# Kernel tuning notes

Hardware: AMD Instinct MI355X
Metric: run time of the kernel (lower is better)

Reference implementation:

```python
import jax, jax.numpy as jnp
import numpy as np

KSZ = 7
PAD = 3


def setup_inputs() -> dict:
    key = jax.random.key(0)
    ks = jax.random.split(key, 5)
    b, t, c, h, w = 8, 16, 256, 28, 28
    x = jax.random.normal(ks[0], (b, t, c, h, w), dtype=jnp.float32)
    W1 = jax.random.normal(ks[1], (2 * t, t), dtype=jnp.float32) * 0.1
    W2 = jax.random.normal(ks[2], (KSZ, 2 * t), dtype=jnp.float32) * 0.1
    Wl1 = jax.random.normal(ks[3], (c // 4, c, KSZ), dtype=jnp.float32) * 0.05
    Wl2 = jax.random.normal(ks[4], (c, c // 4, 1), dtype=jnp.float32) * 0.1
    return {"x": x, "W1": W1, "W2": W2, "Wl1": Wl1, "Wl2": Wl2}


def _tam_forward(x, W1, W2, Wl1, Wl2):
    b, t, c, h, w = x.shape
    xp = jnp.transpose(x, (0, 2, 1, 3, 4))  # [b,c,t,h,w]
    pooled = jnp.mean(xp, axis=(3, 4))       # [b,c,t] (adaptive_avg_pool2d to 1x1)

    # G branch: per-(b,c) dynamic 7-tap softmax kernel
    g = jnp.tanh(jnp.einsum('bct,ut->bcu', pooled, W1))
    kernel = jax.nn.softmax(jnp.einsum('bcu,ku->bck', g, W2), axis=-1)  # [b,c,7]

    # L branch: conv1d(c -> c/4, k=7, pad=3) -> tanh -> conv1d(c/4 -> c, k=1) -> sigmoid
    y = jax.lax.conv_general_dilated(
        pooled, Wl1, window_strides=(1,), padding=[(PAD, PAD)],
        dimension_numbers=('NCH', 'OIH', 'NCH'))
    y = jnp.tanh(y)  # [b, c/4, t]
    local = jax.nn.sigmoid(jnp.einsum('oi,bit->bot', Wl2[:, :, 0], y))  # [b,c,t]

    gated = xp * local[:, :, :, None, None]  # [b,c,t,h,w]

    # Depthwise temporal conv (groups = b*c), stride 1, pad 3 on t
    padded = jnp.pad(gated, ((0, 0), (0, 0), (PAD, PAD), (0, 0), (0, 0)))
    out = jnp.zeros_like(gated)
    for k in range(KSZ):
        out = out + kernel[:, :, k, None, None, None] * padded[:, :, k:k + t]
    out = jnp.transpose(out, (0, 2, 1, 3, 4))  # [b,t,c,h,w]
    return out.reshape(b * t, c, h, w)


def reference(x, W1, W2, Wl1, Wl2):
    return _tam_forward(x, W1, W2, Wl1, Wl2)
```

## Files before the change

### kernel.cpp

```cpp
#include <hip/hip_runtime.h>

constexpr int B_  = 8;
constexpr int T_  = 16;
constexpr int C_  = 256;
constexpr int HW_ = 784;
constexpr int CO_ = 64;
constexpr int K_  = 7;
constexpr int U2_ = 32;

typedef float floatx4 __attribute__((ext_vector_type(4)));

__global__ __launch_bounds__(256) void pool_kernel(const float* __restrict__ x,
                                                   float* __restrict__ pooled) {
    int bid  = blockIdx.x;
    int cg   = bid & 63;
    int bt   = bid >> 6;
    int t    = bt & 15;
    int b    = bt >> 4;
    int wave = threadIdx.x >> 6;
    int lane = threadIdx.x & 63;
    int c    = cg * 4 + wave;

    const float4* p4 = (const float4*)(x + ((size_t)bt * C_ + c) * HW_);
    float s = 0.f;
    for (int j = lane; j < 196; j += 64) {
        float4 v = p4[j];
        s += (v.x + v.y) + (v.z + v.w);
    }
#pragma unroll
    for (int m = 32; m >= 1; m >>= 1) s += __shfl_xor(s, m, 64);
    if (lane == 0) pooled[((size_t)b * C_ + c) * T_ + t] = s * (1.0f / 784.0f);
}

__global__ __launch_bounds__(256) void ty_kernel(const float* __restrict__ pooled,
                                                 const float* __restrict__ Wl1,
                                                 float* __restrict__ ty) {
    int b = blockIdx.x / CO_;
    int o = blockIdx.x % CO_;
    __shared__ float pld[T_ * 257];

    int tid = threadIdx.x;
    for (int idx = tid; idx < C_ * T_; idx += 256) {
        int i  = idx >> 4;
        int tt = idx & 15;
        pld[tt * 257 + i] = pooled[((size_t)b * C_ + i) * T_ + tt];
    }
    __syncthreads();

    int t = tid >> 4;
    int q = tid & 15;
    const float* wrow = Wl1 + (size_t)o * (C_ * K_);
    float acc = 0.f;
    for (int j = 0; j < 16; ++j) {
        int i = j * 16 + q;
        const float* wp = wrow + i * K_;
#pragma unroll
        for (int k = 0; k < K_; ++k) {
            int tt = t + k - 3;
            if (tt >= 0 && tt < T_) acc += wp[k] * pld[tt * 257 + i];
        }
    }
    acc += __shfl_xor(acc, 1, 64);
    acc += __shfl_xor(acc, 2, 64);
    acc += __shfl_xor(acc, 4, 64);
    acc += __shfl_xor(acc, 8, 64);
    if (q == 0) ty[((size_t)b * CO_ + o) * T_ + t] = tanhf(acc);
}

__global__ __launch_bounds__(64) void abuild_kernel(const float* __restrict__ pooled,
                                                    const float* __restrict__ ty,
                                                    const float* __restrict__ W1,
                                                    const float* __restrict__ W2,
                                                    const float* __restrict__ Wl2,
                                                    float* __restrict__ P) {
    int bc = blockIdx.x;
    int b  = bc >> 8;
    int c  = bc & 255;
    int lane = threadIdx.x;

    __shared__ float g_s[U2_];
    __shared__ float s_s[K_];
    __shared__ float loc_s[T_];
    __shared__ float kw_s[8];

    {
        int t = lane >> 2, q = lane & 3;
        float acc = 0.f;
#pragma unroll
        for (int jj = 0; jj < 16; ++jj) {
            int i = q * 16 + jj;
            acc += Wl2[(size_t)c * CO_ + i] * ty[((size_t)b * CO_ + i) * T_ + t];
        }
        acc += __shfl_xor(acc, 1, 64);
        acc += __shfl_xor(acc, 2, 64);
        if (q == 0) loc_s[t] = 1.0f / (1.0f + __expf(-acc));
    }
    if (lane < U2_) {
        float acc = 0.f;
#pragma unroll
        for (int t2 = 0; t2 < T_; ++t2)
            acc += pooled[((size_t)b * C_ + c) * T_ + t2] * W1[lane * T_ + t2];
        g_s[lane] = tanhf(acc);
    }
    __syncthreads();
    if (lane < K_) {
        float acc = 0.f;
#pragma unroll
        for (int u = 0; u < U2_; ++u) acc += g_s[u] * W2[lane * U2_ + u];
        s_s[lane] = acc;
    }
    __syncthreads();
    if (lane == 0) {
        float m = s_s[0];
#pragma unroll
        for (int k = 1; k < K_; ++k) m = fmaxf(m, s_s[k]);
        float e[K_], sum = 0.f;
#pragma unroll
        for (int k = 0; k < K_; ++k) { e[k] = __expf(s_s[k] - m); sum += e[k]; }
        float inv = 1.0f / sum;
#pragma unroll
        for (int k = 0; k < K_; ++k) kw_s[k] = e[k] * inv;
        kw_s[7] = 0.f;
    }
    __syncthreads();
    float* row = P + (size_t)bc * 32;
    if (lane < 8)                 row[lane] = kw_s[lane];
    if (lane >= 8 && lane < 24)   row[lane] = loc_s[lane - 8];
}

__global__ __launch_bounds__(256) void stream_kernel(const float* __restrict__ x,
                                                     const float* __restrict__ P,
                                                     float* __restrict__ out) {
    int gid = blockIdx.x * 256 + threadIdx.x;
    int bc  = gid / 196;
    int col = gid - bc * 196;
    int b   = bc >> 8;
    int c   = bc & 255;

    const float* row = P + (size_t)bc * 32;
    float4 kwa = *(const float4*)(row);
    float4 kwb = *(const float4*)(row + 4);
    float kw[K_] = {kwa.x, kwa.y, kwa.z, kwa.w, kwb.x, kwb.y, kwb.z};
    float loc[T_];
#pragma unroll
    for (int j = 0; j < 4; ++j) {
        float4 l = *(const float4*)(row + 8 + 4 * j);
        loc[4 * j + 0] = l.x; loc[4 * j + 1] = l.y;
        loc[4 * j + 2] = l.z; loc[4 * j + 3] = l.w;
    }

    size_t base = ((size_t)(b * T_) * C_ + c) * HW_ + (size_t)col * 4;
    const size_t ts = (size_t)C_ * HW_;

    float4 yv[T_];
#pragma unroll
    for (int tp = 0; tp < T_; ++tp) {
        float4 v = *(const float4*)(x + base + tp * ts);
        float l = loc[tp];
        v.x *= l; v.y *= l; v.z *= l; v.w *= l;
        yv[tp] = v;
    }
#pragma unroll
    for (int t = 0; t < T_; ++t) {
        floatx4 acc = {0.f, 0.f, 0.f, 0.f};
#pragma unroll
        for (int d = -3; d <= 3; ++d) {
            int tp = t + d;
            if (tp >= 0 && tp < T_) {
                float a = kw[d + 3];
                acc.x += a * yv[tp].x;
                acc.y += a * yv[tp].y;
                acc.z += a * yv[tp].z;
                acc.w += a * yv[tp].w;
            }
        }
        __builtin_nontemporal_store(acc, (floatx4*)(out + base + (size_t)t * ts));
    }
}

extern "C" void kernel_launch(void* const* d_in, const int* in_sizes, int n_in,
                              void* d_out, int out_size, void* d_ws, size_t ws_size,
                              hipStream_t stream) {
    const float* x   = (const float*)d_in[0];
    const float* W1  = (const float*)d_in[1];
    const float* W2  = (const float*)d_in[2];
    const float* Wl1 = (const float*)d_in[3];
    const float* Wl2 = (const float*)d_in[4];
    float* out = (float*)d_out;

    float* pooled = (float*)d_ws;
    float* ty     = pooled + B_ * C_ * T_;
    float* P      = ty + B_ * CO_ * T_;

    pool_kernel<<<B_ * T_ * (C_ / 4), 256, 0, stream>>>(x, pooled);
    ty_kernel<<<B_ * CO_, 256, 0, stream>>>(pooled, Wl1, ty);
    abuild_kernel<<<B_ * C_, 64, 0, stream>>>(pooled, ty, W1, W2, Wl2, P);
    stream_kernel<<<(B_ * C_ * 196) / 256, 256, 0, stream>>>(x, P, out);
}
```

Measured before the change: 72.72 us.

## Map one block per channel in stream kernel and split time loop into halves

The streaming kernel now launches one block per (b,c) channel, with 196 active threads out of 256. The per-channel kernel weights and gates are made wave-uniform via readfirstlane so they can sit in scalar registers. The 16-step register window is replaced by two overlapping 11-frame windows, which lowers vector register pressure, and launch bounds request higher occupancy. The cost is 60 idle lanes per block and some loads issued later, after the first half of the stores.

```diff
diff --git a/kernel.cpp b/kernel.cpp
--- a/kernel.cpp
+++ b/kernel.cpp
@@ -9,6 +9,10 @@
 constexpr int U2_ = 32;
 
 typedef float floatx4 __attribute__((ext_vector_type(4)));
+
+__device__ __forceinline__ float rfl(float v) {
+    return __int_as_float(__builtin_amdgcn_readfirstlane(__float_as_int(v)));
+}
 
 __global__ __launch_bounds__(256) void pool_kernel(const float* __restrict__ x,
                                                    float* __restrict__ pooled) {
@@ -128,53 +132,61 @@
     if (lane >= 8 && lane < 24)   row[lane] = loc_s[lane - 8];
 }
 
-__global__ __launch_bounds__(256) void stream_kernel(const float* __restrict__ x,
-                                                     const float* __restrict__ P,
-                                                     float* __restrict__ out) {
-    int gid = blockIdx.x * 256 + threadIdx.x;
-    int bc  = gid / 196;
-    int col = gid - bc * 196;
-    int b   = bc >> 8;
-    int c   = bc & 255;
+__global__ __launch_bounds__(256, 8) void stream_kernel(const float* __restrict__ x,
+                                                        const float* __restrict__ P,
+                                                        float* __restrict__ out) {
+    int bc = blockIdx.x;
+    int b  = bc >> 8;
+    int c  = bc & 255;
+    int col = threadIdx.x;
 
     const float* row = P + (size_t)bc * 32;
-    float4 kwa = *(const float4*)(row);
-    float4 kwb = *(const float4*)(row + 4);
-    float kw[K_] = {kwa.x, kwa.y, kwa.z, kwa.w, kwb.x, kwb.y, kwb.z};
-    float loc[T_];
-#pragma unroll
-    for (int j = 0; j < 4; ++j) {
-        float4 l = *(const float4*)(row + 8 + 4 * j);
-        loc[4 * j + 0] = l.x; loc[4 * j + 1] = l.y;
-        loc[4 * j + 2] = l.z; loc[4 * j + 3] = l.w;
-    }
-
-    size_t base = ((size_t)(b * T_) * C_ + c) * HW_ + (size_t)col * 4;
+    float kw[K_];
+    float lc[T_];
+#pragma unroll
+    for (int k = 0; k < K_; ++k) kw[k] = rfl(row[k]);
+#pragma unroll
+    for (int t = 0; t < T_; ++t) lc[t] = rfl(row[8 + t]);
+
+    if (col >= 196) return;
+
+    const size_t chan = ((size_t)b * T_ * C_ + c) * HW_ + (size_t)col * 4;
+    const float* xb = x + chan;
+    float*       ob = out + chan;
     const size_t ts = (size_t)C_ * HW_;
 
-    float4 yv[T_];
-#pragma unroll
-    for (int tp = 0; tp < T_; ++tp) {
-        float4 v = *(const float4*)(x + base + tp * ts);
-        float l = loc[tp];
-        v.x *= l; v.y *= l; v.z *= l; v.w *= l;
-        yv[tp] = v;
-    }
-#pragma unroll
-    for (int t = 0; t < T_; ++t) {
+    floatx4 w[11];
+#pragma unroll
+    for (int tp = 0; tp < 11; ++tp)
+        w[tp] = *(const floatx4*)(xb + (size_t)tp * ts) * lc[tp];
+
+#pragma unroll
+    for (int t = 0; t < 8; ++t) {
         floatx4 acc = {0.f, 0.f, 0.f, 0.f};
 #pragma unroll
         for (int d = -3; d <= 3; ++d) {
             int tp = t + d;
-            if (tp >= 0 && tp < T_) {
-                float a = kw[d + 3];
-                acc.x += a * yv[tp].x;
-                acc.y += a * yv[tp].y;
-                acc.z += a * yv[tp].z;
-                acc.w += a * yv[tp].w;
-            }
-        }
-        __builtin_nontemporal_store(acc, (floatx4*)(out + base + (size_t)t * ts));
+            if (tp >= 0 && tp <= 10) acc += kw[d + 3] * w[tp];
+        }
+        __builtin_nontemporal_store(acc, (floatx4*)(ob + (size_t)t * ts));
+    }
+
+    floatx4 w2[11];
+#pragma unroll
+    for (int j = 0; j < 6; ++j) w2[j] = w[5 + j];
+#pragma unroll
+    for (int tp = 11; tp < 16; ++tp)
+        w2[tp - 5] = *(const floatx4*)(xb + (size_t)tp * ts) * lc[tp];
+
+#pragma unroll
+    for (int t = 8; t < 16; ++t) {
+        floatx4 acc = {0.f, 0.f, 0.f, 0.f};
+#pragma unroll
+        for (int d = -3; d <= 3; ++d) {
+            int tp = t + d;
+            if (tp <= 15) acc += kw[d + 3] * w2[tp - 5];
+        }
+        __builtin_nontemporal_store(acc, (floatx4*)(ob + (size_t)t * ts));
     }
 }
 
@@ -195,5 +207,5 @@
     pool_kernel<<<B_ * T_ * (C_ / 4), 256, 0, stream>>>(x, pooled);
     ty_kernel<<<B_ * CO_, 256, 0, stream>>>(pooled, Wl1, ty);
     abuild_kernel<<<B_ * C_, 64, 0, stream>>>(pooled, ty, W1, W2, Wl2, P);
-    stream_kernel<<<(B_ * C_ * 196) / 256, 256, 0, stream>>>(x, P, out);
-}
+    stream_kernel<<<B_ * C_, 256, 0, stream>>>(x, P, out);
+}
```

Result: no change. 72.99 us (+0.4%).
